# Kernel optimization log

Hardware: AMD Instinct MI355X
Metric: run time of the kernel (lower is better)

## Reference

```python
import jax, jax.numpy as jnp
import numpy as np

N_NODES = 50000


def setup_inputs() -> dict:
    key = jax.random.key(0)
    k1, k2, k3 = jax.random.split(key, 3)
    x = jax.random.normal(k1, (N_NODES, 128), dtype=jnp.float32)
    edge_index = jax.random.randint(k2, (2, 800000), 0, N_NODES, dtype=jnp.int64)
    weight = jax.random.normal(k3, (128, 128), dtype=jnp.float32) * (1.0 / np.sqrt(128))
    bias = jnp.zeros((128,), dtype=jnp.float32)
    return {"x": x, "edge_index": edge_index, "weight": weight, "bias": bias}


def reference(x, edge_index, weight, bias):
    # GCNConv (PyG defaults): add self-loops, sym-normalize, linear, scatter-add, bias; then ReLU.
    N = x.shape[0]
    self_loops = jnp.arange(N, dtype=edge_index.dtype)
    row = jnp.concatenate([edge_index[0], self_loops])  # source nodes [E+N]
    col = jnp.concatenate([edge_index[1], self_loops])  # target nodes [E+N]

    # degree over targets (edge weights are all ones), includes self-loops -> deg >= 1
    deg = jax.ops.segment_sum(jnp.ones_like(col, dtype=x.dtype), col, num_segments=N)
    dinv = jax.lax.rsqrt(deg)
    norm = dinv[row] * dinv[col]  # [E+N]

    h = x @ weight  # [N, nhid] linear transform before propagation
    msgs = h[row] * norm[:, None]  # gather + scale, [E+N, nhid]
    out = jax.ops.segment_sum(msgs, col, num_segments=N) + bias  # scatter-add aggregate
    return jax.nn.relu(out)
```

## Files before the change

### kernel.cpp

```cpp
#include <hip/hip_runtime.h>

#define NFEAT 128
#define CAP 64
#define NROLE 4
#define CHUNK 2048

typedef __attribute__((ext_vector_type(8))) short short8;
typedef __attribute__((ext_vector_type(4))) float f32x4;
typedef __attribute__((ext_vector_type(4))) float f32x4v;
typedef __attribute__((ext_vector_type(2))) float f32x2v;
typedef __attribute__((ext_vector_type(4))) int i32x4;

__device__ inline short f2bf(float f) {
    unsigned u = __builtin_bit_cast(unsigned, f);
    u += 0x7FFFu + ((u >> 16) & 1u);
    return (short)(u >> 16);
}
__device__ inline float bf2f(unsigned short u) {
    return __builtin_bit_cast(float, ((unsigned)u) << 16);
}

__global__ void prep_kernel(const float* __restrict__ W, unsigned short* __restrict__ Wt,
                            unsigned int* __restrict__ cnt, int N) {
    int i = blockIdx.x * 256 + threadIdx.x;
    if (i < N) cnt[i] = 0u;
    if (i < NFEAT * NFEAT) {
        int k = i >> 7, n = i & 127;
        Wt[n * NFEAT + k] = (unsigned short)f2bf(W[k * NFEAT + n]);
    }
}

__global__ void __launch_bounds__(256)
gemm_countfill_kernel(const float* __restrict__ x,
                      const unsigned short* __restrict__ Wt,
                      unsigned short* __restrict__ h, int N, int gb,
                      const int* __restrict__ row, const int* __restrict__ col,
                      int E, unsigned int* __restrict__ cnt,
                      unsigned short* __restrict__ bucket) {
    __shared__ unsigned short tile[4][16][136];
    int bid = blockIdx.x;

    if (bid >= gb) {
        int k = bid - gb;
        int role = bid & (NROLE - 1);
        int q = k >> 2;
        int rlo = (int)((long long)N * role / NROLE);
        int rhi = (int)((long long)N * (role + 1) / NROLE);
        int ebase = q * CHUNK + (int)threadIdx.x * 4;
        #pragma unroll
        for (int half = 0; half < 2; ++half) {
            int e = ebase + half * 1024;
            if (e + 3 < E) {
                i32x4 c4 = *(const i32x4*)(col + e);
                i32x4 r4 = *(const i32x4*)(row + e);
                #pragma unroll
                for (int u = 0; u < 4; ++u) {
                    int c = c4[u];
                    if (c >= rlo && c < rhi) {
                        unsigned int t = atomicAdd(&cnt[c], 1u);
                        if (t < CAP) bucket[(size_t)c * CAP + t] = (unsigned short)r4[u];
                    }
                }
            }
        }
        return;
    }

    int wave = threadIdx.x >> 6;
    int lane = threadIdx.x & 63;
    int li = lane & 15;
    int kg = lane >> 4;
    int m0 = bid * 64 + wave * 16;
    int arow = m0 + li;
    int srow = (arow < N) ? arow : (N - 1);

    f32x4 acc[8];
    #pragma unroll
    for (int nt = 0; nt < 8; ++nt) acc[nt] = (f32x4){0.f, 0.f, 0.f, 0.f};

    #pragma unroll
    for (int ks = 0; ks < 4; ++ks) {
        const f32x4v* xp = (const f32x4v*)(x + (size_t)srow * NFEAT + ks * 32 + kg * 8);
        f32x4v f0 = __builtin_nontemporal_load(xp);
        f32x4v f1 = __builtin_nontemporal_load(xp + 1);
        short8 a;
        a[0] = f2bf(f0.x); a[1] = f2bf(f0.y); a[2] = f2bf(f0.z); a[3] = f2bf(f0.w);
        a[4] = f2bf(f1.x); a[5] = f2bf(f1.y); a[6] = f2bf(f1.z); a[7] = f2bf(f1.w);
        #pragma unroll
        for (int nt = 0; nt < 8; ++nt) {
            short8 b = *(const short8*)(Wt + (size_t)(nt * 16 + li) * NFEAT + ks * 32 + kg * 8);
            acc[nt] = __builtin_amdgcn_mfma_f32_16x16x32_bf16(a, b, acc[nt], 0, 0, 0);
        }
    }

    #pragma unroll
    for (int r = 0; r < 4; ++r) {
        #pragma unroll
        for (int nt = 0; nt < 8; ++nt)
            tile[wave][kg * 4 + r][nt * 16 + li] = (unsigned short)f2bf(acc[nt][r]);
    }
    __syncthreads();

    int rr = lane >> 2;
    int orow = m0 + rr;
    #pragma unroll
    for (int cc = 0; cc < 4; ++cc) {
        int chunk = cc * 4 + (lane & 3);
        if (orow < N) {
            short8 v = *(const short8*)&tile[wave][rr][chunk * 8];
            *(short8*)(h + (size_t)orow * NFEAT + chunk * 8) = v;
        }
    }
}

__global__ void aggregate_kernel(const unsigned short* __restrict__ h,
                                 const unsigned short* __restrict__ bucket,
                                 const unsigned int* __restrict__ cnt,
                                 const float* __restrict__ bias,
                                 float* __restrict__ out, int N) {
    int wid = threadIdx.x >> 6;
    int lane = threadIdx.x & 63;
    int c = blockIdx.x * 4 + wid;
    if (c >= N) return;
    int grp = lane >> 4;
    int li = lane & 15;
    int col0 = li * 8;
    int n = (int)cnt[c];
    float dc = rsqrtf((float)(n + 1));
    if (n > CAP) n = CAP;

    int myidx = (lane < n) ? (int)bucket[(size_t)c * CAP + lane] : c;
    float mydr = (lane < n) ? rsqrtf((float)(cnt[myidx] + 1u)) : 0.f;

    float acc[8];
    if (grp == 0) {
        short8 v = *(const short8*)(h + (size_t)c * NFEAT + col0);
        #pragma unroll
        for (int i = 0; i < 8; ++i) acc[i] = bf2f((unsigned short)v[i]) * dc;
    } else {
        #pragma unroll
        for (int i = 0; i < 8; ++i) acc[i] = 0.f;
    }

    for (int j = 0; j < n; j += 16) {
        int idx[4];
        float dr[4];
        short8 v[4];
        #pragma unroll
        for (int k = 0; k < 4; ++k) {
            int e = j + k * 4 + grp;
            idx[k] = __shfl(myidx, e, 64);
            dr[k] = __shfl(mydr, e, 64);
        }
        #pragma unroll
        for (int k = 0; k < 4; ++k)
            v[k] = *(const short8*)(h + (size_t)idx[k] * NFEAT + col0);
        #pragma unroll
        for (int k = 0; k < 4; ++k) {
            #pragma unroll
            for (int i = 0; i < 8; ++i) acc[i] += bf2f((unsigned short)v[k][i]) * dr[k];
        }
    }

    #pragma unroll
    for (int i = 0; i < 8; ++i) {
        acc[i] += __shfl_xor(acc[i], 16, 64);
        acc[i] += __shfl_xor(acc[i], 32, 64);
    }

    float a0, a1;
    switch (grp) {
        case 0: a0 = acc[0]; a1 = acc[1]; break;
        case 1: a0 = acc[2]; a1 = acc[3]; break;
        case 2: a0 = acc[4]; a1 = acc[5]; break;
        default: a0 = acc[6]; a1 = acc[7]; break;
    }
    float dc2 = dc;
    const float2* bp = (const float2*)(bias + col0 + grp * 2);
    float2 b = *bp;
    f32x2v o;
    o.x = fmaxf(a0 * dc2 + b.x, 0.f);
    o.y = fmaxf(a1 * dc2 + b.y, 0.f);
    __builtin_nontemporal_store(o, (f32x2v*)(out + (size_t)c * NFEAT + col0 + grp * 2));
}

extern "C" void kernel_launch(void* const* d_in, const int* in_sizes, int n_in,
                              void* d_out, int out_size, void* d_ws, size_t ws_size,
                              hipStream_t stream) {
    const float* x    = (const float*)d_in[0];
    const int*   ei   = (const int*)d_in[1];
    const float* W    = (const float*)d_in[2];
    const float* bias = (const float*)d_in[3];
    float* out = (float*)d_out;

    int N = in_sizes[0] / NFEAT;
    int E = in_sizes[1] / 2;
    const int* row = ei;
    const int* col = ei + E;

    char* ws = (char*)d_ws;
    size_t o = 0;
    unsigned int*   cnt    = (unsigned int*)(ws + o);   o += (size_t)N * 4;
    unsigned short* Wt     = (unsigned short*)(ws + o); o += (size_t)NFEAT * NFEAT * 2;
    unsigned short* bucket = (unsigned short*)(ws + o); o += (size_t)N * CAP * 2;
    unsigned short* h      = (unsigned short*)(ws + o);

    int nb = (N + 255) / 256;
    int gb = (N + 63) / 64;
    int per_role = (E + CHUNK - 1) / CHUNK;
    int cb = NROLE * per_role;

    prep_kernel<<<nb, 256, 0, stream>>>(W, Wt, cnt, N);
    gemm_countfill_kernel<<<gb + cb, 256, 0, stream>>>(x, Wt, h, N, gb,
                                                       row, col, E, cnt, bucket);
    aggregate_kernel<<<(N + 3) / 4, 256, 0, stream>>>(h, bucket, cnt, bias, out, N);
}
```

Before: 100.7 us.

## Split aggregation across four column-slice blocks per node and load row lazily

The aggregate kernel now launches four blocks per node group, each handling a 32-column slice. Within a slice, eight lane groups of 8 each gather 4 bf16 values per neighbor, and results are reduced with three xor-shuffles. This raises parallelism and shrinks per-thread register state, but the bucket indices and degree rsqrt are now recomputed four times per node. The count/fill path also reads row only for edges that fall in the block's node range instead of vector-loading it unconditionally, which saves bandwidth but turns that read into scattered scalar loads.

```diff
diff --git a/kernel.cpp b/kernel.cpp
--- a/kernel.cpp
+++ b/kernel.cpp
@@ -8,8 +8,8 @@
 typedef __attribute__((ext_vector_type(8))) short short8;
 typedef __attribute__((ext_vector_type(4))) float f32x4;
 typedef __attribute__((ext_vector_type(4))) float f32x4v;
-typedef __attribute__((ext_vector_type(2))) float f32x2v;
 typedef __attribute__((ext_vector_type(4))) int i32x4;
+typedef __attribute__((ext_vector_type(4))) unsigned short u16x4;
 
 __device__ inline short f2bf(float f) {
     unsigned u = __builtin_bit_cast(unsigned, f);
@@ -52,13 +52,13 @@
             int e = ebase + half * 1024;
             if (e + 3 < E) {
                 i32x4 c4 = *(const i32x4*)(col + e);
-                i32x4 r4 = *(const i32x4*)(row + e);
                 #pragma unroll
                 for (int u = 0; u < 4; ++u) {
                     int c = c4[u];
                     if (c >= rlo && c < rhi) {
+                        int r = row[e + u];
                         unsigned int t = atomicAdd(&cnt[c], 1u);
-                        if (t < CAP) bucket[(size_t)c * CAP + t] = (unsigned short)r4[u];
+                        if (t < CAP) bucket[(size_t)c * CAP + t] = (unsigned short)r;
                     }
                 }
             }
@@ -120,11 +120,12 @@
                                  float* __restrict__ out, int N) {
     int wid = threadIdx.x >> 6;
     int lane = threadIdx.x & 63;
-    int c = blockIdx.x * 4 + wid;
+    int slice = blockIdx.x & 3;
+    int c = (blockIdx.x >> 2) * 4 + wid;
     if (c >= N) return;
-    int grp = lane >> 4;
-    int li = lane & 15;
-    int col0 = li * 8;
+    int g = lane >> 3;
+    int li = lane & 7;
+    int cb = slice * 32 + li * 4;
     int n = (int)cnt[c];
     float dc = rsqrtf((float)(n + 1));
     if (n > CAP) n = CAP;
@@ -132,56 +133,42 @@
     int myidx = (lane < n) ? (int)bucket[(size_t)c * CAP + lane] : c;
     float mydr = (lane < n) ? rsqrtf((float)(cnt[myidx] + 1u)) : 0.f;
 
-    float acc[8];
-    if (grp == 0) {
-        short8 v = *(const short8*)(h + (size_t)c * NFEAT + col0);
-        #pragma unroll
-        for (int i = 0; i < 8; ++i) acc[i] = bf2f((unsigned short)v[i]) * dc;
+    float acc[4];
+    if (g == 0) {
+        u16x4 v = *(const u16x4*)(h + (size_t)c * NFEAT + cb);
+        #pragma unroll
+        for (int i = 0; i < 4; ++i) acc[i] = bf2f(v[i]) * dc;
     } else {
         #pragma unroll
-        for (int i = 0; i < 8; ++i) acc[i] = 0.f;
-    }
-
-    for (int j = 0; j < n; j += 16) {
-        int idx[4];
-        float dr[4];
-        short8 v[4];
-        #pragma unroll
-        for (int k = 0; k < 4; ++k) {
-            int e = j + k * 4 + grp;
-            idx[k] = __shfl(myidx, e, 64);
-            dr[k] = __shfl(mydr, e, 64);
-        }
-        #pragma unroll
-        for (int k = 0; k < 4; ++k)
-            v[k] = *(const short8*)(h + (size_t)idx[k] * NFEAT + col0);
-        #pragma unroll
-        for (int k = 0; k < 4; ++k) {
-            #pragma unroll
-            for (int i = 0; i < 8; ++i) acc[i] += bf2f((unsigned short)v[k][i]) * dr[k];
-        }
-    }
-
-    #pragma unroll
-    for (int i = 0; i < 8; ++i) {
+        for (int i = 0; i < 4; ++i) acc[i] = 0.f;
+    }
+
+    for (int j = 0; j < n; j += 8) {
+        int e = j + g;
+        int idx = __shfl(myidx, e & 63, 64);
+        float dr = __shfl(mydr, e & 63, 64);
+        dr = (e < n) ? dr : 0.f;
+        u16x4 v = *(const u16x4*)(h + (size_t)idx * NFEAT + cb);
+        #pragma unroll
+        for (int i = 0; i < 4; ++i) acc[i] += bf2f(v[i]) * dr;
+    }
+
+    #pragma unroll
+    for (int i = 0; i < 4; ++i) {
+        acc[i] += __shfl_xor(acc[i], 8, 64);
         acc[i] += __shfl_xor(acc[i], 16, 64);
         acc[i] += __shfl_xor(acc[i], 32, 64);
     }
 
-    float a0, a1;
-    switch (grp) {
-        case 0: a0 = acc[0]; a1 = acc[1]; break;
-        case 1: a0 = acc[2]; a1 = acc[3]; break;
-        case 2: a0 = acc[4]; a1 = acc[5]; break;
-        default: a0 = acc[6]; a1 = acc[7]; break;
-    }
-    float dc2 = dc;
-    const float2* bp = (const float2*)(bias + col0 + grp * 2);
-    float2 b = *bp;
-    f32x2v o;
-    o.x = fmaxf(a0 * dc2 + b.x, 0.f);
-    o.y = fmaxf(a1 * dc2 + b.y, 0.f);
-    __builtin_nontemporal_store(o, (f32x2v*)(out + (size_t)c * NFEAT + col0 + grp * 2));
+    if (g == 0) {
+        f32x4v b = *(const f32x4v*)(bias + cb);
+        f32x4v o;
+        o.x = fmaxf(acc[0] * dc + b.x, 0.f);
+        o.y = fmaxf(acc[1] * dc + b.y, 0.f);
+        o.z = fmaxf(acc[2] * dc + b.z, 0.f);
+        o.w = fmaxf(acc[3] * dc + b.w, 0.f);
+        __builtin_nontemporal_store(o, (f32x4v*)(out + (size_t)c * NFEAT + cb));
+    }
 }
 
 extern "C" void kernel_launch(void* const* d_in, const int* in_sizes, int n_in,
@@ -213,5 +200,7 @@
     prep_kernel<<<nb, 256, 0, stream>>>(W, Wt, cnt, N);
     gemm_countfill_kernel<<<gb + cb, 256, 0, stream>>>(x, Wt, h, N, gb,
                                                        row, col, E, cnt, bucket);
-    aggregate_kernel<<<(N + 3) / 4, 256, 0, stream>>>(h, bucket, cnt, bias, out, N);
-}
+
+    int bps = (N + 3) / 4;
+    aggregate_kernel<<<bps * 4, 256, 0, stream>>>(h, bucket, cnt, bias, out, N);
+}
```

Result: slower. 145.0 us (+44.0%).
